# Kernel tuning notes

Measured on AMD Instinct MI355X. Metric: run time of the kernel, lower is better.

The kernel has to match this reference:

```python
import jax, jax.numpy as jnp
import numpy as np

PATCH = 256
N = 50000
HC = 256  # height // PATCH
WC = 256  # width // PATCH

def _gauss_kernel():
    # GaussianSmoothing(channels=1, kernel_size=3, sigma=0.5)
    g = np.exp(-(((np.arange(3, dtype=np.float64) - 1.0) / 0.5) ** 2) / 2.0) / (0.5 * np.sqrt(2 * np.pi))
    k = np.outer(g, g)
    k = k / k.sum()
    return jnp.asarray(k, jnp.float32).reshape(1, 1, 3, 3)

def setup_inputs() -> dict:
    key = jax.random.key(0)
    ks = jax.random.split(key, 12)
    h = jax.random.normal(ks[0], (N, 1024), jnp.float32)
    # unique grid cells per patch (row-major), scaled back to pixel coords
    idx = jnp.arange(N, dtype=jnp.int64 if jax.config.jax_enable_x64 else jnp.int32)
    gx = idx % WC
    gy = idx // WC
    coords = jnp.stack([gx * PATCH, gy * PATCH], axis=1)
    eps = jax.random.normal(ks[1], (1, 1, HC, WC), jnp.float32)
    s = 0.02
    W1 = jax.random.normal(ks[2], (512, 1024), jnp.float32) * s
    b1 = jnp.zeros((512,), jnp.float32)
    W2a = jax.random.normal(ks[3], (256, 512), jnp.float32) * s
    b2a = jnp.zeros((256,), jnp.float32)
    W2b = jax.random.normal(ks[4], (256, 512), jnp.float32) * s
    b2b = jnp.zeros((256,), jnp.float32)
    W3 = jax.random.normal(ks[5], (2, 256), jnp.float32) * s
    b3 = jnp.zeros((2,), jnp.float32)
    Wc = jax.random.normal(ks[6], (2, 512), jnp.float32) * s
    bc = jnp.zeros((2,), jnp.float32)
    kernel = _gauss_kernel()
    return {"h": h, "coords": coords, "eps": eps,
            "W1": W1, "b1": b1, "W2a": W2a, "b2a": b2a, "W2b": W2b, "b2b": b2b,
            "W3": W3, "b3": b3, "Wc": Wc, "bc": bc, "kernel": kernel,
            "height": 65536, "width": 65536, "slide_label": 1}

def reference(h, coords, eps, W1, b1, W2a, b2a, W2b, b2b, W3, b3, Wc, bc, kernel, height, width, slide_label):
    hc, wc = height // PATCH, width // PATCH
    x = jax.nn.relu(h @ W1.T + b1)                      # [N,512] (dropout = eval identity)
    fa = jax.nn.sigmoid(x @ W2a.T + b2a)                # [N,256]
    fb = jnp.tanh(x @ W2b.T + b2b)                      # [N,256]
    params = (fa * fb) @ W3.T + b3                      # [N,2] -> (mu, logvar) per patch
    gx = coords[:, 0] // PATCH
    gy = coords[:, 1] // PATCH
    mu = jnp.zeros((1, hc, wc), x.dtype).at[0, gy, gx].set(params[:, 0])
    logvar = jnp.zeros((1, hc, wc), x.dtype).at[0, gy, gx].set(params[:, 1])
    prior_mu = jnp.array([-5.0, 0.0], x.dtype)[slide_label]
    prior_lv = jnp.array([-1.0, 3.0], x.dtype)[slide_label]
    kl_div = (prior_lv - logvar) / 2.0 + (logvar ** 2 + (prior_mu - mu) ** 2) / (2.0 * prior_lv ** 2) - 0.5
    mu_pad = jnp.pad(mu, ((0, 0), (1, 1), (1, 1)))[None]          # [1,1,hc+2,wc+2]
    mu_sm = jax.lax.conv_general_dilated(mu_pad, kernel, (1, 1), 'VALID')  # [1,1,hc,wc]
    samples = mu_sm + eps * jnp.exp(0.5 * logvar)                  # reparameterize, broadcast to [1,1,hc,wc]
    A = jax.nn.sigmoid(samples[0])                                 # [1,hc,wc]
    patch_A = A[0, gy, gx][None]                                   # gather -> [1,N]
    M = (patch_A @ x) / patch_A.sum()                              # [1,512]
    logits = M @ Wc.T + bc                                         # [1,n_classes]
    y_probs = jax.nn.softmax(logits, axis=1)
    top_idx = jax.lax.top_k(y_probs[:, 1], 1)[1]                   # top_k=1
    top_instance = logits[top_idx]                                 # [1,n_classes]
    Y_hat = jnp.argmax(top_instance, axis=1, keepdims=True)
    Y_prob = jax.nn.softmax(top_instance, axis=1)
    return (top_instance, Y_prob, Y_hat, kl_div, y_probs, patch_A)
```

## Files before the change

kernel.cpp:

```cpp
#include <hip/hip_runtime.h>
#include <hip/hip_bf16.h>
#include <cstdint>
#include <cstddef>

#define NPATCH 50000
#define GC 256

typedef __bf16 bf16x8 __attribute__((ext_vector_type(8)));
typedef float  f32x4  __attribute__((ext_vector_type(4)));
typedef float  f32x8  __attribute__((ext_vector_type(8)));

static constexpr size_t XB_OFF    = 0;
static constexpr size_t XB_BYTES  = (size_t)50048 * 512 * 2;
static constexpr size_t W1B_OFF   = XB_OFF + XB_BYTES;
static constexpr size_t W1B_BYTES = (size_t)512 * 1024 * 2;
static constexpr size_t W2AB_OFF  = W1B_OFF + W1B_BYTES;
static constexpr size_t W2X_BYTES = (size_t)256 * 512 * 2;
static constexpr size_t W2BB_OFF  = W2AB_OFF + W2X_BYTES;
static constexpr size_t MUG_OFF   = W2BB_OFF + W2X_BYTES;
static constexpr size_t LVG_OFF   = MUG_OFF + (size_t)65536 * 4;
static constexpr size_t AG_OFF    = LVG_OFF + (size_t)65536 * 4;
static constexpr size_t MPART_OFF = AG_OFF + (size_t)65536 * 4;
static constexpr size_t SUMA_OFF  = MPART_OFF + (size_t)512 * 4;
static constexpr size_t ZERO_BYTES = SUMA_OFF + 4 - MUG_OFF;

__device__ __forceinline__ unsigned short f2bf(float f) {
  union { float f; uint32_t u; } v; v.f = f;
  uint32_t u = v.u;
  uint32_t r = (u + 0x7FFFu + ((u >> 16) & 1u)) >> 16;
  return (unsigned short)r;
}
__device__ __forceinline__ float bf2f(uint32_t bits16) {
  union { uint32_t u; float f; } v; v.u = bits16 << 16; return v.f;
}
__device__ __forceinline__ unsigned short cvt_bf16(float f) {
  __bf16 b = (__bf16)f;
  return __builtin_bit_cast(unsigned short, b);
}
__device__ __forceinline__ void gld16(const void* g, void* l) {
  __builtin_amdgcn_global_load_lds(
      (const __attribute__((address_space(1))) void*)g,
      (__attribute__((address_space(3))) void*)l, 16, 0, 0);
}
__device__ __forceinline__ bf16x8 cvt8(const float4& f0, const float4& f1) {
  f32x8 fv;
  fv[0]=f0.x; fv[1]=f0.y; fv[2]=f0.z; fv[3]=f0.w;
  fv[4]=f1.x; fv[5]=f1.y; fv[6]=f1.z; fv[7]=f1.w;
  return __builtin_convertvector(fv, bf16x8);
}

__global__ void convert_weights(const float* __restrict__ W1,
                                const float* __restrict__ W2a,
                                const float* __restrict__ W2b,
                                unsigned short* __restrict__ W1b,
                                unsigned short* __restrict__ W2ab,
                                unsigned short* __restrict__ W2bb) {
  int i = blockIdx.x * 256 + threadIdx.x;
  if (i < 512 * 1024) W1b[i] = f2bf(W1[i]);
  if (i < 256 * 512) { W2ab[i] = f2bf(W2a[i]); W2bb[i] = f2bf(W2b[i]); }
}

__global__ __launch_bounds__(256, 2) void gemm1(
    const float* __restrict__ h, const unsigned short* __restrict__ W1b,
    const float* __restrict__ b1, unsigned short* __restrict__ xb) {
  __shared__ __align__(16) unsigned short As[2][128 * 32];
  __shared__ __align__(16) unsigned short Bs[2][256 * 32];

  const int t  = threadIdx.x;
  const int l  = t & 63;
  const int w  = t >> 6;
  const int wr = w >> 1;
  const int wc = w & 1;
  const int g  = l >> 4;
  const int lr = l & 15;

  const int i   = blockIdx.x;
  const int xcd = i & 7;
  const int pos = i >> 3;
  const int v   = (xcd < 6 ? xcd * 98 : 6 * 98 + (xcd - 6) * 97) + pos;
  const int rt  = v >> 1;
  const int ct  = v & 1;
  const int rowBase = rt * 128;
  const int colBase = ct * 256;

  const int ar = t >> 2;
  const int aj = t & 3;
  int gr0 = rowBase + ar;       if (gr0 >= NPATCH) gr0 = NPATCH - 1;
  int gr1 = rowBase + 64 + ar;  if (gr1 >= NPATCH) gr1 = NPATCH - 1;
  const float* asrc0 = h + (size_t)gr0 * 1024 + aj * 8;
  const float* asrc1 = h + (size_t)gr1 * 1024 + aj * 8;
  const int aslot = aj ^ ((ar >> 1) & 3);
  const int adst0 = ar * 32 + aslot * 8;
  const int adst1 = (64 + ar) * 32 + aslot * 8;

  const int bj = (t & 3) ^ ((t >> 3) & 3);
  const unsigned short* bsrc[4];
#pragma unroll
  for (int r = 0; r < 4; ++r)
    bsrc[r] = W1b + (size_t)(colBase + r * 64 + (t >> 2)) * 1024 + bj * 8;

  const int rslot = (g ^ ((lr >> 1) & 3)) * 8;

  f32x4 acc[4][8];
#pragma unroll
  for (int mm = 0; mm < 4; ++mm)
#pragma unroll
    for (int nn = 0; nn < 8; ++nn) acc[mm][nn] = (f32x4){0.f, 0.f, 0.f, 0.f};

  float4 s00, s01, s10, s11;
  {
#pragma unroll
    for (int r = 0; r < 4; ++r) gld16(bsrc[r], &Bs[0][r * 2048 + t * 8]);
    float4 t00 = *(const float4*)(asrc0 + 0);
    float4 t01 = *(const float4*)(asrc0 + 4);
    float4 t10 = *(const float4*)(asrc1 + 0);
    float4 t11 = *(const float4*)(asrc1 + 4);
    *(bf16x8*)&As[0][adst0] = cvt8(t00, t01);
    *(bf16x8*)&As[0][adst1] = cvt8(t10, t11);
    s00 = *(const float4*)(asrc0 + 32);
    s01 = *(const float4*)(asrc0 + 36);
    s10 = *(const float4*)(asrc1 + 32);
    s11 = *(const float4*)(asrc1 + 36);
  }
  asm volatile("s_waitcnt lgkmcnt(0)\n\ts_barrier" ::: "memory");

  int cur = 0;
  for (int kt = 0; kt < 32; ++kt) {
    const int kb = (kt + 1 <= 31) ? (kt + 1) : 31;
#pragma unroll
    for (int r = 0; r < 4; ++r)
      gld16(bsrc[r] + kb * 32, &Bs[cur ^ 1][r * 2048 + t * 8]);
    __builtin_amdgcn_sched_barrier(0);
    *(bf16x8*)&As[cur ^ 1][adst0] = cvt8(s00, s01);
    *(bf16x8*)&As[cur ^ 1][adst1] = cvt8(s10, s11);
    const int ka = (kt + 2 <= 31) ? (kt + 2) : 31;
    s00 = *(const float4*)(asrc0 + ka * 32);
    s01 = *(const float4*)(asrc0 + ka * 32 + 4);
    s10 = *(const float4*)(asrc1 + ka * 32);
    s11 = *(const float4*)(asrc1 + ka * 32 + 4);
    __builtin_amdgcn_sched_barrier(0);
    bf16x8 af[4], bfr[8];
#pragma unroll
    for (int mm = 0; mm < 4; ++mm)
      af[mm] = *(const bf16x8*)&As[cur][(wr * 64 + mm * 16 + lr) * 32 + rslot];
#pragma unroll
    for (int nn = 0; nn < 8; ++nn)
      bfr[nn] = *(const bf16x8*)&Bs[cur][(wc * 128 + nn * 16 + lr) * 32 + rslot];
#pragma unroll
    for (int mm = 0; mm < 4; ++mm)
#pragma unroll
      for (int nn = 0; nn < 8; ++nn)
        acc[mm][nn] = __builtin_amdgcn_mfma_f32_16x16x32_bf16(af[mm], bfr[nn], acc[mm][nn], 0, 0, 0);
    asm volatile("s_waitcnt vmcnt(4) lgkmcnt(0)\n\ts_barrier" ::: "memory");
    cur ^= 1;
  }

  float b1v[8];
#pragma unroll
  for (int nn = 0; nn < 8; ++nn) b1v[nn] = b1[colBase + wc * 128 + nn * 16 + lr];
#pragma unroll
  for (int mm = 0; mm < 4; ++mm) {
    const int rb0 = rowBase + wr * 64 + mm * 16 + g * 4;
#pragma unroll
    for (int r = 0; r < 4; ++r) {
      const int row = rb0 + r;
      if (row < NPATCH) {
        unsigned short* xrow = xb + (size_t)row * 512 + colBase + wc * 128;
#pragma unroll
        for (int nn = 0; nn < 8; ++nn) {
          float vv = acc[mm][nn][r] + b1v[nn];
          vv = vv > 0.f ? vv : 0.f;
          xrow[nn * 16 + lr] = cvt_bf16(vv);
        }
      }
    }
  }
}

__global__ __launch_bounds__(256, 2) void gemm2(
    const unsigned short* __restrict__ xb,
    const unsigned short* __restrict__ W2ab, const unsigned short* __restrict__ W2bb,
    const float* __restrict__ b2a, const float* __restrict__ b2b,
    const float* __restrict__ W3, const float* __restrict__ b3,
    const int* __restrict__ coords,
    float* __restrict__ mug, float* __restrict__ lvg) {
  __shared__ __align__(16) unsigned short xs[64 * 40];
  __shared__ __align__(16) unsigned short was[256 * 40];
  __shared__ __align__(16) unsigned short wbs[256 * 40];
  __shared__ float pmu_s[4][64];
  __shared__ float plv_s[4][64];

  const int t = threadIdx.x;
  const int l = t & 63;
  const int w = t >> 6;
  const int g = l >> 4, lr = l & 15;
  const int rowBase = blockIdx.x * 64;

  f32x4 aa[4][4], ab[4][4];
#pragma unroll
  for (int m = 0; m < 4; ++m)
#pragma unroll
    for (int n = 0; n < 4; ++n) {
      aa[m][n] = (f32x4){0.f, 0.f, 0.f, 0.f};
      ab[m][n] = (f32x4){0.f, 0.f, 0.f, 0.f};
    }

  const int xrow = t >> 2;
  const int xc0  = (t & 3) * 8;
  const int grow = rowBase + xrow;
  const bool xval = grow < NPATCH;

  for (int kt = 0; kt < 16; ++kt) {
    const int k0 = kt * 32;
    __syncthreads();
    if (xval) {
      *(int4*)&xs[xrow * 40 + xc0] = *(const int4*)(xb + (size_t)grow * 512 + k0 + xc0);
    } else {
      int4 z = {0, 0, 0, 0};
      *(int4*)&xs[xrow * 40 + xc0] = z;
    }
#pragma unroll
    for (int j = 0; j < 4; ++j) {
      int rrow = (t >> 2) + 64 * j;
      *(int4*)&was[rrow * 40 + xc0] = *(const int4*)(W2ab + (size_t)rrow * 512 + k0 + xc0);
      *(int4*)&wbs[rrow * 40 + xc0] = *(const int4*)(W2bb + (size_t)rrow * 512 + k0 + xc0);
    }
    __syncthreads();

    bf16x8 af[4], ba[4], bb[4];
#pragma unroll
    for (int m = 0; m < 4; ++m)
      af[m] = *(const bf16x8*)&xs[(m * 16 + lr) * 40 + g * 8];
#pragma unroll
    for (int n = 0; n < 4; ++n) {
      int brow = w * 64 + n * 16 + lr;
      ba[n] = *(const bf16x8*)&was[brow * 40 + g * 8];
      bb[n] = *(const bf16x8*)&wbs[brow * 40 + g * 8];
    }
#pragma unroll
    for (int m = 0; m < 4; ++m)
#pragma unroll
      for (int n = 0; n < 4; ++n) {
        aa[m][n] = __builtin_amdgcn_mfma_f32_16x16x32_bf16(af[m], ba[n], aa[m][n], 0, 0, 0);
        ab[m][n] = __builtin_amdgcn_mfma_f32_16x16x32_bf16(af[m], bb[n], ab[m][n], 0, 0, 0);
      }
  }

  float b2av[4], b2bv[4], w30v[4], w31v[4];
#pragma unroll
  for (int n = 0; n < 4; ++n) {
    int col = w * 64 + n * 16 + lr;
    b2av[n] = b2a[col]; b2bv[n] = b2b[col];
    w30v[n] = W3[col];  w31v[n] = W3[256 + col];
  }
#pragma unroll
  for (int m = 0; m < 4; ++m) {
#pragma unroll
    for (int r = 0; r < 4; ++r) {
      float pm = 0.f, pl = 0.f;
#pragma unroll
      for (int n = 0; n < 4; ++n) {
        float a = 1.f / (1.f + __expf(-(aa[m][n][r] + b2av[n])));
        float b = tanhf(ab[m][n][r] + b2bv[n]);
        float p = a * b;
        pm += p * w30v[n];
        pl += p * w31v[n];
      }
#pragma unroll
      for (int d = 1; d < 16; d <<= 1) {
        pm += __shfl_xor(pm, d, 64);
        pl += __shfl_xor(pl, d, 64);
      }
      if (lr == 0) {
        pmu_s[w][m * 16 + g * 4 + r] = pm;
        plv_s[w][m * 16 + g * 4 + r] = pl;
      }
    }
  }
  __syncthreads();
  if (t < 64) {
    float mu = pmu_s[0][t] + pmu_s[1][t] + pmu_s[2][t] + pmu_s[3][t] + b3[0];
    float lv = plv_s[0][t] + plv_s[1][t] + plv_s[2][t] + plv_s[3][t] + b3[1];
    int row = rowBase + t;
    if (row < NPATCH) {
      int gx = coords[2 * row] >> 8;
      int gy = coords[2 * row + 1] >> 8;
      int cell = gy * GC + gx;
      mug[cell] = mu;
      lvg[cell] = lv;
    }
  }
}

__global__ void grid_ops(const float* __restrict__ mug, const float* __restrict__ lvg,
                         const float* __restrict__ eps, const float* __restrict__ kern,
                         const int* __restrict__ slide, float* __restrict__ Ag,
                         float* __restrict__ out_kl) {
  int cell = blockIdx.x * 256 + threadIdx.x;
  int iy = cell >> 8, ix = cell & 255;
  float mu = mug[cell], lv = lvg[cell];
  int sl = slide[0];
  float pm  = (sl == 0) ? -5.0f : 0.0f;
  float plv = (sl == 0) ? -1.0f : 3.0f;
  float d = pm - mu;
  out_kl[cell] = (plv - lv) * 0.5f + (lv * lv + d * d) / (2.0f * plv * plv) - 0.5f;
  float s = 0.f;
#pragma unroll
  for (int dy = 0; dy < 3; ++dy) {
#pragma unroll
    for (int dx = 0; dx < 3; ++dx) {
      int y = iy + dy - 1, x = ix + dx - 1;
      if (y >= 0 && y < GC && x >= 0 && x < GC)
        s += mug[y * GC + x] * kern[dy * 3 + dx];
    }
  }
  float sample = s + eps[cell] * __expf(0.5f * lv);
  Ag[cell] = 1.f / (1.f + __expf(-sample));
}

__global__ __launch_bounds__(256) void patch_pass(
    const float* __restrict__ Ag, const int* __restrict__ coords,
    const unsigned short* __restrict__ xb, float* __restrict__ out_pA,
    float* __restrict__ Mpart, float* __restrict__ sumA) {
  __shared__ float als[256];
  __shared__ float swave[4];
  const int t = threadIdx.x;
  const int base = blockIdx.x * 256;
  const int row = base + t;
  float a = 0.f;
  if (row < NPATCH) {
    int gx = coords[2 * row] >> 8;
    int gy = coords[2 * row + 1] >> 8;
    a = Ag[gy * GC + gx];
    out_pA[row] = a;
  }
  als[t] = a;
  float sa = a;
#pragma unroll
  for (int d = 1; d < 64; d <<= 1) sa += __shfl_xor(sa, d, 64);
  if ((t & 63) == 0) swave[t >> 6] = sa;
  __syncthreads();
  if (t == 0) atomicAdd(sumA, swave[0] + swave[1] + swave[2] + swave[3]);

  const int nrows = min(256, NPATCH - base);
  float m0 = 0.f, m1 = 0.f;
  for (int r = 0; r < nrows; ++r) {
    float av = als[r];
    const uint32_t* p = (const uint32_t*)(xb + (size_t)(base + r) * 512);
    uint32_t v = p[t];
    m0 += av * bf2f(v & 0xFFFFu);
    m1 += av * bf2f(v >> 16);
  }
  atomicAdd(&Mpart[t * 2 + 0], m0);
  atomicAdd(&Mpart[t * 2 + 1], m1);
}

__global__ void finalize(const float* __restrict__ Mpart, const float* __restrict__ sumA,
                         const float* __restrict__ Wc, const float* __restrict__ bc,
                         float* __restrict__ out) {
  const int t = threadIdx.x;
  float s = sumA[0];
  float l0 = 0.f, l1 = 0.f;
#pragma unroll
  for (int j = 0; j < 8; ++j) {
    int c = t * 8 + j;
    float m = Mpart[c] / s;
    l0 += m * Wc[c];
    l1 += m * Wc[512 + c];
  }
#pragma unroll
  for (int d = 1; d < 64; d <<= 1) {
    l0 += __shfl_xor(l0, d, 64);
    l1 += __shfl_xor(l1, d, 64);
  }
  if (t == 0) {
    l0 += bc[0]; l1 += bc[1];
    float mx = fmaxf(l0, l1);
    float e0 = __expf(l0 - mx), e1 = __expf(l1 - mx);
    float inv = 1.f / (e0 + e1);
    float p0 = e0 * inv, p1 = e1 * inv;
    out[0] = l0; out[1] = l1;
    out[2] = p0; out[3] = p1;
    out[4] = (l1 > l0) ? 1.0f : 0.0f;
    out[65541] = p0; out[65542] = p1;
  }
}

extern "C" void kernel_launch(void* const* d_in, const int* in_sizes, int n_in,
                              void* d_out, int out_size, void* d_ws, size_t ws_size,
                              hipStream_t stream) {
  const float* h      = (const float*)d_in[0];
  const int*   coords = (const int*)d_in[1];
  const float* eps    = (const float*)d_in[2];
  const float* W1     = (const float*)d_in[3];
  const float* b1     = (const float*)d_in[4];
  const float* W2a    = (const float*)d_in[5];
  const float* b2a    = (const float*)d_in[6];
  const float* W2b    = (const float*)d_in[7];
  const float* b2b    = (const float*)d_in[8];
  const float* W3     = (const float*)d_in[9];
  const float* b3     = (const float*)d_in[10];
  const float* Wc     = (const float*)d_in[11];
  const float* bc     = (const float*)d_in[12];
  const float* kern   = (const float*)d_in[13];
  const int*   slide  = (const int*)d_in[16];
  float* out = (float*)d_out;
  char*  ws  = (char*)d_ws;

  unsigned short* xb   = (unsigned short*)(ws + XB_OFF);
  unsigned short* W1b  = (unsigned short*)(ws + W1B_OFF);
  unsigned short* W2ab = (unsigned short*)(ws + W2AB_OFF);
  unsigned short* W2bb = (unsigned short*)(ws + W2BB_OFF);
  float* mug   = (float*)(ws + MUG_OFF);
  float* lvg   = (float*)(ws + LVG_OFF);
  float* Ag    = (float*)(ws + AG_OFF);
  float* Mpart = (float*)(ws + MPART_OFF);
  float* sumA  = (float*)(ws + SUMA_OFF);

  hipMemsetAsync(ws + MUG_OFF, 0, ZERO_BYTES, stream);

  convert_weights<<<2048, 256, 0, stream>>>(W1, W2a, W2b, W1b, W2ab, W2bb);
  gemm1<<<782, 256, 0, stream>>>(h, W1b, b1, xb);
  gemm2<<<782, 256, 0, stream>>>(xb, W2ab, W2bb, b2a, b2b, W3, b3, coords, mug, lvg);
  grid_ops<<<256, 256, 0, stream>>>(mug, lvg, eps, kern, slide, Ag, out + 5);
  patch_pass<<<196, 256, 0, stream>>>(Ag, coords, xb, out + 65543, Mpart, sumA);
  finalize<<<1, 64, 0, stream>>>(Mpart, sumA, Wc, bc, out);
}
```

Before: 204.1 us.

## Enlarge gemm1 tile to 256x256 with 512 threads and triple-buffered B

Reworks the first GEMM to use 256x256 output tiles computed by 8 waves (2x4) in 512-thread blocks, halving the grid. B tiles become triple-buffered with async global-to-LDS loads issued two steps ahead. The MFMA work is split into two half-phases with barriers and s_setprio so loads and compute interleave. This aims for more reuse per LDS load and better latency hiding, at the cost of more LDS per block, possibly lower occupancy, and a single wave of 392 blocks whose tail may be uneven.

Result: faster. 190.9 us (-6.5%).

```diff
diff --git a/kernel.cpp b/kernel.cpp
--- a/kernel.cpp
+++ b/kernel.cpp
@@ -60,117 +60,138 @@
   if (i < 256 * 512) { W2ab[i] = f2bf(W2a[i]); W2bb[i] = f2bf(W2b[i]); }
 }
 
-__global__ __launch_bounds__(256, 2) void gemm1(
+__global__ __launch_bounds__(512, 2) void gemm1(
     const float* __restrict__ h, const unsigned short* __restrict__ W1b,
     const float* __restrict__ b1, unsigned short* __restrict__ xb) {
-  __shared__ __align__(16) unsigned short As[2][128 * 32];
-  __shared__ __align__(16) unsigned short Bs[2][256 * 32];
+  __shared__ __align__(16) unsigned short lds[40960];
+  unsigned short* const A0 = lds;
+  unsigned short* const A1 = lds + 8192;
+  unsigned short* const B0 = lds + 16384;
+  unsigned short* const B1 = lds + 24576;
+  unsigned short* const B2 = lds + 32768;
 
   const int t  = threadIdx.x;
   const int l  = t & 63;
   const int w  = t >> 6;
-  const int wr = w >> 1;
-  const int wc = w & 1;
+  const int wm = w >> 2;
+  const int wn = w & 3;
   const int g  = l >> 4;
   const int lr = l & 15;
 
   const int i   = blockIdx.x;
   const int xcd = i & 7;
   const int pos = i >> 3;
-  const int v   = (xcd < 6 ? xcd * 98 : 6 * 98 + (xcd - 6) * 97) + pos;
+  const int v   = xcd * 49 + pos;
   const int rt  = v >> 1;
   const int ct  = v & 1;
-  const int rowBase = rt * 128;
+  const int rowBase = rt * 256;
   const int colBase = ct * 256;
 
-  const int ar = t >> 2;
-  const int aj = t & 3;
-  int gr0 = rowBase + ar;       if (gr0 >= NPATCH) gr0 = NPATCH - 1;
-  int gr1 = rowBase + 64 + ar;  if (gr1 >= NPATCH) gr1 = NPATCH - 1;
-  const float* asrc0 = h + (size_t)gr0 * 1024 + aj * 8;
-  const float* asrc1 = h + (size_t)gr1 * 1024 + aj * 8;
-  const int aslot = aj ^ ((ar >> 1) & 3);
-  const int adst0 = ar * 32 + aslot * 8;
-  const int adst1 = (64 + ar) * 32 + aslot * 8;
+  const int tr = t >> 1;
+  const int hh = t & 1;
+  int gr = rowBase + tr; if (gr >= NPATCH) gr = NPATCH - 1;
+  const float* ah = h + (size_t)gr * 1024 + hh * 16;
+  const int sw  = (tr >> 1) & 3;
+  const int aw0 = tr * 32 + ((hh * 2)     ^ sw) * 8;
+  const int aw1 = tr * 32 + ((hh * 2 + 1) ^ sw) * 8;
 
   const int bj = (t & 3) ^ ((t >> 3) & 3);
-  const unsigned short* bsrc[4];
-#pragma unroll
-  for (int r = 0; r < 4; ++r)
-    bsrc[r] = W1b + (size_t)(colBase + r * 64 + (t >> 2)) * 1024 + bj * 8;
-
-  const int rslot = (g ^ ((lr >> 1) & 3)) * 8;
-
-  f32x4 acc[4][8];
-#pragma unroll
-  for (int mm = 0; mm < 4; ++mm)
-#pragma unroll
-    for (int nn = 0; nn < 8; ++nn) acc[mm][nn] = (f32x4){0.f, 0.f, 0.f, 0.f};
-
-  float4 s00, s01, s10, s11;
+  const unsigned short* bh  = W1b + (size_t)(colBase + (t >> 2)) * 1024 + bj * 8;
+  const unsigned short* bh2 = bh + (size_t)128 * 1024;
+  const int bd0 = t * 8;
+  const int bd1 = 4096 + t * 8;
+
+  const int rs = (g ^ ((lr >> 1) & 3)) * 8;
+  const int abase = (wm * 128 + lr) * 32 + rs;
+  const int bbase = (wn * 64 + lr) * 32 + rs;
+
+  f32x4 acc[8][4];
+#pragma unroll
+  for (int m = 0; m < 8; ++m)
+#pragma unroll
+    for (int n = 0; n < 4; ++n) acc[m][n] = (f32x4){0.f, 0.f, 0.f, 0.f};
+
+  unsigned short *pAr = A0, *pAw = A1;
+  unsigned short *pBr = B0, *pBr1 = B1, *pBw = B2;
+
+  float4 q0, q1, q2, q3;
   {
-#pragma unroll
-    for (int r = 0; r < 4; ++r) gld16(bsrc[r], &Bs[0][r * 2048 + t * 8]);
-    float4 t00 = *(const float4*)(asrc0 + 0);
-    float4 t01 = *(const float4*)(asrc0 + 4);
-    float4 t10 = *(const float4*)(asrc1 + 0);
-    float4 t11 = *(const float4*)(asrc1 + 4);
-    *(bf16x8*)&As[0][adst0] = cvt8(t00, t01);
-    *(bf16x8*)&As[0][adst1] = cvt8(t10, t11);
-    s00 = *(const float4*)(asrc0 + 32);
-    s01 = *(const float4*)(asrc0 + 36);
-    s10 = *(const float4*)(asrc1 + 32);
-    s11 = *(const float4*)(asrc1 + 36);
+    gld16(bh, pBr + bd0); gld16(bh2, pBr + bd1);
+    float4 f0 = *(const float4*)(ah + 0);
+    float4 f1 = *(const float4*)(ah + 4);
+    float4 f2 = *(const float4*)(ah + 8);
+    float4 f3 = *(const float4*)(ah + 12);
+    *(bf16x8*)(pAr + aw0) = cvt8(f0, f1);
+    *(bf16x8*)(pAr + aw1) = cvt8(f2, f3);
+    q0 = *(const float4*)(ah + 32);
+    q1 = *(const float4*)(ah + 36);
+    q2 = *(const float4*)(ah + 40);
+    q3 = *(const float4*)(ah + 44);
+    gld16(bh + 32, pBr1 + bd0); gld16(bh2 + 32, pBr1 + bd1);
   }
   asm volatile("s_waitcnt lgkmcnt(0)\n\ts_barrier" ::: "memory");
 
-  int cur = 0;
   for (int kt = 0; kt < 32; ++kt) {
-    const int kb = (kt + 1 <= 31) ? (kt + 1) : 31;
-#pragma unroll
-    for (int r = 0; r < 4; ++r)
-      gld16(bsrc[r] + kb * 32, &Bs[cur ^ 1][r * 2048 + t * 8]);
+    const int ka = ((kt + 2 <= 31) ? (kt + 2) : 31) * 32;
+    bf16x8 af[4], bf[4];
+#pragma unroll
+    for (int m = 0; m < 4; ++m)
+      af[m] = *(const bf16x8*)(pAr + abase + m * 512);
+#pragma unroll
+    for (int n = 0; n < 4; ++n)
+      bf[n] = *(const bf16x8*)(pBr + bbase + n * 512);
+    *(bf16x8*)(pAw + aw0) = cvt8(q0, q1);
+    *(bf16x8*)(pAw + aw1) = cvt8(q2, q3);
+    q0 = *(const float4*)(ah + ka + 0);
+    q1 = *(const float4*)(ah + ka + 4);
+    q2 = *(const float4*)(ah + ka + 8);
+    q3 = *(const float4*)(ah + ka + 12);
     __builtin_amdgcn_sched_barrier(0);
-    *(bf16x8*)&As[cur ^ 1][adst0] = cvt8(s00, s01);
-    *(bf16x8*)&As[cur ^ 1][adst1] = cvt8(s10, s11);
-    const int ka = (kt + 2 <= 31) ? (kt + 2) : 31;
-    s00 = *(const float4*)(asrc0 + ka * 32);
-    s01 = *(const float4*)(asrc0 + ka * 32 + 4);
-    s10 = *(const float4*)(asrc1 + ka * 32);
-    s11 = *(const float4*)(asrc1 + ka * 32 + 4);
+    __builtin_amdgcn_s_barrier();
+    __builtin_amdgcn_s_setprio(1);
+#pragma unroll
+    for (int m = 0; m < 4; ++m)
+#pragma unroll
+      for (int n = 0; n < 4; ++n)
+        acc[m][n] = __builtin_amdgcn_mfma_f32_16x16x32_bf16(af[m], bf[n], acc[m][n], 0, 0, 0);
+    __builtin_amdgcn_s_setprio(0);
+    __builtin_amdgcn_s_barrier();
+#pragma unroll
+    for (int m = 0; m < 4; ++m)
+      af[m] = *(const bf16x8*)(pAr + abase + (m + 4) * 512);
+    gld16(bh + ka, pBw + bd0);
+    gld16(bh2 + ka, pBw + bd1);
     __builtin_amdgcn_sched_barrier(0);
-    bf16x8 af[4], bfr[8];
-#pragma unroll
-    for (int mm = 0; mm < 4; ++mm)
-      af[mm] = *(const bf16x8*)&As[cur][(wr * 64 + mm * 16 + lr) * 32 + rslot];
-#pragma unroll
-    for (int nn = 0; nn < 8; ++nn)
-      bfr[nn] = *(const bf16x8*)&Bs[cur][(wc * 128 + nn * 16 + lr) * 32 + rslot];
-#pragma unroll
-    for (int mm = 0; mm < 4; ++mm)
-#pragma unroll
-      for (int nn = 0; nn < 8; ++nn)
-        acc[mm][nn] = __builtin_amdgcn_mfma_f32_16x16x32_bf16(af[mm], bfr[nn], acc[mm][nn], 0, 0, 0);
-    asm volatile("s_waitcnt vmcnt(4) lgkmcnt(0)\n\ts_barrier" ::: "memory");
-    cur ^= 1;
-  }
-
-  float b1v[8];
-#pragma unroll
-  for (int nn = 0; nn < 8; ++nn) b1v[nn] = b1[colBase + wc * 128 + nn * 16 + lr];
-#pragma unroll
-  for (int mm = 0; mm < 4; ++mm) {
-    const int rb0 = rowBase + wr * 64 + mm * 16 + g * 4;
+    __builtin_amdgcn_s_barrier();
+    __builtin_amdgcn_s_setprio(1);
+#pragma unroll
+    for (int m = 0; m < 4; ++m)
+#pragma unroll
+      for (int n = 0; n < 4; ++n)
+        acc[m + 4][n] = __builtin_amdgcn_mfma_f32_16x16x32_bf16(af[m], bf[n], acc[m + 4][n], 0, 0, 0);
+    __builtin_amdgcn_s_setprio(0);
+    asm volatile("s_waitcnt vmcnt(6) lgkmcnt(0)\n\ts_barrier" ::: "memory");
+    unsigned short* tA = pAr; pAr = pAw; pAw = tA;
+    unsigned short* tB = pBr; pBr = pBr1; pBr1 = pBw; pBw = tB;
+  }
+  asm volatile("s_waitcnt vmcnt(0) lgkmcnt(0)" ::: "memory");
+
+  float b1v[4];
+#pragma unroll
+  for (int n = 0; n < 4; ++n) b1v[n] = b1[colBase + wn * 64 + n * 16 + lr];
+#pragma unroll
+  for (int m = 0; m < 8; ++m) {
+    const int rb0 = rowBase + wm * 128 + m * 16 + g * 4;
 #pragma unroll
     for (int r = 0; r < 4; ++r) {
       const int row = rb0 + r;
       if (row < NPATCH) {
-        unsigned short* xrow = xb + (size_t)row * 512 + colBase + wc * 128;
-#pragma unroll
-        for (int nn = 0; nn < 8; ++nn) {
-          float vv = acc[mm][nn][r] + b1v[nn];
+        unsigned short* xrow = xb + (size_t)row * 512 + colBase + wn * 64;
+#pragma unroll
+        for (int n = 0; n < 4; ++n) {
+          float vv = acc[m][n][r] + b1v[n];
           vv = vv > 0.f ? vv : 0.f;
-          xrow[nn * 16 + lr] = cvt_bf16(vv);
+          xrow[n * 16 + lr] = cvt_bf16(vv);
         }
       }
     }
@@ -420,7 +441,7 @@
   hipMemsetAsync(ws + MUG_OFF, 0, ZERO_BYTES, stream);
 
   convert_weights<<<2048, 256, 0, stream>>>(W1, W2a, W2b, W1b, W2ab, W2bb);
-  gemm1<<<782, 256, 0, stream>>>(h, W1b, b1, xb);
+  gemm1<<<392, 512, 0, stream>>>(h, W1b, b1, xb);
   gemm2<<<782, 256, 0, stream>>>(xb, W2ab, W2bb, b2a, b2b, W3, b3, coords, mug, lvg);
   grid_ops<<<256, 256, 0, stream>>>(mug, lvg, eps, kern, slide, Ag, out + 5);
   patch_pass<<<196, 256, 0, stream>>>(Ag, coords, xb, out + 65543, Mpart, sumA);
```
